# Performance work log

Measured on AMD Instinct MI355X. Metric: run time of the kernel, lower is better.

## Reference

```python
import jax, jax.numpy as jnp
import numpy as np

N_NODES = 100000
E2 = 1600000
E3 = 1600000
ES = 100000
HID = 64


def _mlp_3x3(x_in, W1, b1, W2, b2):
    # x_in: [E, d_in] -> mobility [E, 3, 3]
    h = jax.nn.relu(x_in @ W1 + b1)
    out = h @ W2 + b2  # [E, 9]
    return out.reshape(-1, 3, 3)


def setup_inputs() -> dict:
    key = jax.random.key(0)
    ks = jax.random.split(key, 20)
    inp = {}
    inp["x"] = jax.random.normal(ks[0], (N_NODES, 3), dtype=jnp.float32)
    inp["edge_2body"] = jax.random.randint(ks[1], (2, E2), 0, N_NODES)
    inp["edge_3body"] = jax.random.randint(ks[2], (3, E3), 0, N_NODES)
    inp["edge_2bodySelf"] = jax.random.randint(ks[3], (2, ES), 0, N_NODES)
    inp["edge_1body"] = jax.random.randint(ks[4], (2, ES), 0, N_NODES)
    inp["edge_attr_2body"] = jax.random.normal(ks[5], (E2, 3), dtype=jnp.float32)
    inp["edge_attr_3body"] = jax.random.normal(ks[6], (E3, 3), dtype=jnp.float32)
    inp["edge_attr_2bodySelf"] = jax.random.normal(ks[7], (ES, 3), dtype=jnp.float32)
    inp["edge_attr_1body"] = jax.random.normal(ks[8], (ES, 3), dtype=jnp.float32)
    s = 0.1
    # nn_2body: 3 -> HID -> 9
    inp["W1_2b"] = jax.random.normal(ks[9], (3, HID), dtype=jnp.float32) * s
    inp["b1_2b"] = jnp.zeros((HID,), jnp.float32)
    inp["W2_2b"] = jax.random.normal(ks[10], (HID, 9), dtype=jnp.float32) * s
    inp["b2_2b"] = jnp.zeros((9,), jnp.float32)
    # nn_3body: 6 -> HID -> 9
    inp["W1_3b"] = jax.random.normal(ks[11], (6, HID), dtype=jnp.float32) * s
    inp["b1_3b"] = jnp.zeros((HID,), jnp.float32)
    inp["W2_3b"] = jax.random.normal(ks[12], (HID, 9), dtype=jnp.float32) * s
    inp["b2_3b"] = jnp.zeros((9,), jnp.float32)
    # nn_self: 3 -> HID -> 9
    inp["W1_s"] = jax.random.normal(ks[13], (3, HID), dtype=jnp.float32) * s
    inp["b1_s"] = jnp.zeros((HID,), jnp.float32)
    inp["W2_s"] = jax.random.normal(ks[14], (HID, 9), dtype=jnp.float32) * s
    inp["b2_s"] = jnp.zeros((9,), jnp.float32)
    return inp


def reference(x, edge_2body, edge_3body, edge_2bodySelf, edge_1body,
              edge_attr_2body, edge_attr_3body, edge_attr_2bodySelf, edge_attr_1body,
              W1_2b, b1_2b, W2_2b, b2_2b,
              W1_3b, b1_3b, W2_3b, b2_3b,
              W1_s, b1_s, W2_s, b2_s):
    n = x.shape[0]
    # ---- 2-body: gather -> MLP -> per-edge 3x3 matvec -> scatter-add ----
    d2 = x[edge_2body[0]] - x[edge_2body[1]]  # xj - xi, [E2,3]
    mob2 = _mlp_3x3(d2, W1_2b, b1_2b, W2_2b, b2_2b)
    y2 = jnp.einsum('eij,ej->ei', mob2, edge_attr_2body)
    v2 = jax.ops.segment_sum(y2, edge_2body[1], num_segments=n)
    # ---- 3-body ----
    xj = x[edge_3body[0]]
    xk = x[edge_3body[1]]
    xi = x[edge_3body[2]]
    d3 = jnp.concatenate((xk - xj, xi - xk), axis=1)  # [E3,6]
    mob3 = _mlp_3x3(d3, W1_3b, b1_3b, W2_3b, b2_3b)
    y3 = jnp.einsum('eij,ej->ei', mob3, edge_attr_3body)
    v3 = jax.ops.segment_sum(y3, edge_3body[2], num_segments=n)
    # ---- 2-body self ----
    ds = x[edge_2bodySelf[0]] - x[edge_2bodySelf[1]]
    mobs = _mlp_3x3(ds, W1_s, b1_s, W2_s, b2_s)
    ys = jnp.einsum('eij,ej->ei', mobs, edge_attr_2bodySelf)
    vs = jax.ops.segment_sum(ys, edge_2bodySelf[1], num_segments=n)
    # edge_1body / edge_attr_1body unused in original forward
    return v2 + v3 + vs
```

## Files before the change

kernel.cpp:

```cpp
#include <hip/hip_runtime.h>


constexpr int HIDDEN = 64;
constexpr int NB_MAX = 256;
constexpr int NPB_SHIFT = 9;
constexpr int NPB = 1 << NPB_SHIFT;
constexpr int SSPLIT = 8;
constexpr int TILE_F = NPB * 3;
constexpr int TILE_F4 = TILE_F / 4;
constexpr int NET_SLOT = 1024;
constexpr int NET_USED = 640;

typedef _Float16 h2_t __attribute__((ext_vector_type(2)));

__device__ __forceinline__ unsigned packh2(float a, float b) {
    auto h = __builtin_amdgcn_cvt_pkrtz(a, b);
    return __builtin_bit_cast(unsigned, h);
}
__device__ __forceinline__ float fdot2u(unsigned a, unsigned b, float c) {
    h2_t ha = __builtin_bit_cast(h2_t, a);
    h2_t hb = __builtin_bit_cast(h2_t, b);
#if __has_builtin(__builtin_amdgcn_fdot2)
    return __builtin_amdgcn_fdot2(ha, hb, c, false);
#else
    return fmaf((float)ha.x, (float)hb.x, fmaf((float)ha.y, (float)hb.y, c));
#endif
}


__global__ __launch_bounds__(256) void setup_kernel(
    const float* __restrict__ x, int n_nodes, float4* __restrict__ x4,
    int* __restrict__ gcount,
    const float* __restrict__ W1_2b, const float* __restrict__ b1_2b,
    const float* __restrict__ W2_2b, const float* __restrict__ b2_2b,
    const float* __restrict__ W1_s,  const float* __restrict__ b1_s,
    const float* __restrict__ W2_s,  const float* __restrict__ b2_s,
    const float* __restrict__ W1_3b, const float* __restrict__ b1_3b,
    const float* __restrict__ W2_3b, const float* __restrict__ b2_3b,
    unsigned* __restrict__ nets)
{
    const int blk = blockIdx.x;
    const int tid = threadIdx.x;
    if (blk < 3) {
        const float *W1, *b1, *W2, *b2; int din;
        if (blk == 0) { W1 = W1_2b; b1 = b1_2b; W2 = W2_2b; b2 = b2_2b; din = 3; }
        else if (blk == 1) { W1 = W1_s; b1 = b1_s; W2 = W2_s; b2 = b2_s; din = 3; }
        else { W1 = W1_3b; b1 = b1_3b; W2 = W2_3b; b2 = b2_3b; din = 6; }
        unsigned* slot = nets + blk * NET_SLOT;
        float* slotf = (float*)slot;
        if (tid < 64) {
            int hh = tid;
            if (din == 3) {
                slot[hh] = packh2(W1[0 * HIDDEN + hh], W1[1 * HIDDEN + hh]);
                slotf[560 + hh] = W1[2 * HIDDEN + hh];
            } else {
                #pragma unroll
                for (int r = 0; r < 3; ++r)
                    slot[hh * 3 + r] =
                        packh2(W1[(2 * r) * HIDDEN + hh], W1[(2 * r + 1) * HIDDEN + hh]);
            }
            slotf[192 + hh] = b1[hh];
        }
        for (int t = tid; t < 288; t += 256) {
            int hh2 = t / 9, i = t - hh2 * 9;
            slot[256 + t] = packh2(W2[(2 * hh2) * 9 + i], W2[(2 * hh2 + 1) * 9 + i]);
        }
        if (tid < 9) slotf[544 + tid] = b2[tid];
        if (blk == 0) gcount[tid] = 0;
    } else {
        int i = (blk - 3) * 256 + tid;
        if (i < n_nodes)
            x4[i] = make_float4(x[3 * i], x[3 * i + 1], x[3 * i + 2], 0.0f);
    }
}

__global__ __launch_bounds__(256) void p1_edge_kernel(
    const float4* __restrict__ x4,
    const int* __restrict__ e0, long long E0, const float* __restrict__ at0,
    const int* __restrict__ e1, long long E1, const float* __restrict__ at1,
    const int* __restrict__ e2, long long E2, const float* __restrict__ at2,
    int g0, int g1,
    const unsigned* __restrict__ nets,
    float4* __restrict__ records, int* __restrict__ gcount, int cap)
{
    constexpr int BLK = 256;
    constexpr int KPT = 4;

    __shared__ int s_hist[NB_MAX];
    __shared__ int s_base[NB_MAX];
    __shared__ int s_rank[NB_MAX];
    __shared__ unsigned s_net[NET_USED];

    const int blk = blockIdx.x;
    const int* edges; long long E; const float* attr;
    int bidx, nblk, din3;
    const unsigned* wp;
    if (blk < g0)           { edges = e0; E = E0; attr = at0; bidx = blk;          nblk = g0;                 din3 = 1; wp = nets; }
    else if (blk < g0 + g1) { edges = e1; E = E1; attr = at1; bidx = blk - g0;     nblk = g1;                 din3 = 1; wp = nets + NET_SLOT; }
    else                    { edges = e2; E = E2; attr = at2; bidx = blk - g0 - g1; nblk = gridDim.x - g0 - g1; din3 = 0; wp = nets + 2 * NET_SLOT; }

    const int tid = threadIdx.x;
    const long long span = (E + nblk - 1) / nblk;
    const long long lo = (long long)bidx * span;
    const long long hi = (lo + span < E) ? (lo + span) : E;
    if (lo >= E) return;

    for (int i = tid; i < NB_MAX; i += BLK) { s_hist[i] = 0; s_rank[i] = 0; }
    for (int i = tid; i < NET_USED; i += BLK) s_net[i] = wp[i];
    __syncthreads();

    const unsigned* w = s_net;
    const float* wf = (const float*)s_net;

    const long long dstrow = din3 ? E : 2 * E;
    for (long long e = lo + tid; e < hi; e += BLK) {
        int d = edges[dstrow + e];
        atomicAdd(&s_hist[d >> NPB_SHIFT], 1);
    }
    __syncthreads();

    for (int i = tid; i < NB_MAX; i += BLK) {
        int h = s_hist[i];
        s_base[i] = (h > 0) ? atomicAdd(&gcount[i], h) : 0;
    }
    __syncthreads();

    for (long long t0 = lo; t0 < hi; t0 += BLK * KPT) {
        unsigned dp[KPT][3];
        float    d2s[KPT];
        float    a[KPT][3];
        int      dst[KPT];
        bool     valid[KPT];

        #pragma unroll
        for (int u = 0; u < KPT; ++u) {
            long long e = t0 + (long long)u * BLK + tid;
            valid[u] = (e < hi);
            long long ee = valid[u] ? e : lo;
            if (din3) {
                int s = edges[ee];
                int t = edges[E + ee];
                dst[u] = t;
                float4 xs = x4[s];
                float4 xt = x4[t];
                dp[u][0] = packh2(xs.x - xt.x, xs.y - xt.y);
                d2s[u]   = xs.z - xt.z;
                dp[u][1] = 0; dp[u][2] = 0;
            } else {
                int j = edges[ee];
                int k = edges[E + ee];
                int i = edges[2 * E + ee];
                dst[u] = i;
                float4 xj = x4[j];
                float4 xk = x4[k];
                float4 xi = x4[i];
                dp[u][0] = packh2(xk.x - xj.x, xk.y - xj.y);
                dp[u][1] = packh2(xk.z - xj.z, xi.x - xk.x);
                dp[u][2] = packh2(xi.y - xk.y, xi.z - xk.z);
                d2s[u] = 0.f;
            }
            #pragma unroll
            for (int c = 0; c < 3; ++c) a[u][c] = attr[3 * ee + c];
        }

        float acc[KPT][9];
        #pragma unroll
        for (int u = 0; u < KPT; ++u)
            #pragma unroll
            for (int i = 0; i < 9; ++i) acc[u][i] = wf[544 + i];

        if (din3) {
            #pragma unroll 2
            for (int hh2 = 0; hh2 < HIDDEN / 2; ++hh2) {
                const unsigned wA = w[2 * hh2];
                const unsigned wB = w[2 * hh2 + 1];
                const float wcA = wf[560 + 2 * hh2];
                const float wcB = wf[561 + 2 * hh2];
                const float bbA = wf[192 + 2 * hh2];
                const float bbB = wf[193 + 2 * hh2];
                unsigned w2p[9];
                #pragma unroll
                for (int i = 0; i < 9; ++i) w2p[i] = w[256 + hh2 * 9 + i];
                #pragma unroll
                for (int u = 0; u < KPT; ++u) {
                    float preA = fmaf(d2s[u], wcA, fdot2u(dp[u][0], wA, bbA));
                    float preB = fmaf(d2s[u], wcB, fdot2u(dp[u][0], wB, bbB));
                    unsigned h2 = packh2(fmaxf(preA, 0.f), fmaxf(preB, 0.f));
                    #pragma unroll
                    for (int i = 0; i < 9; ++i)
                        acc[u][i] = fdot2u(h2, w2p[i], acc[u][i]);
                }
            }
        } else {
            #pragma unroll 2
            for (int hh2 = 0; hh2 < HIDDEN / 2; ++hh2) {
                const unsigned wA0 = w[(2 * hh2) * 3 + 0];
                const unsigned wA1 = w[(2 * hh2) * 3 + 1];
                const unsigned wA2 = w[(2 * hh2) * 3 + 2];
                const unsigned wB0 = w[(2 * hh2 + 1) * 3 + 0];
                const unsigned wB1 = w[(2 * hh2 + 1) * 3 + 1];
                const unsigned wB2 = w[(2 * hh2 + 1) * 3 + 2];
                const float bbA = wf[192 + 2 * hh2];
                const float bbB = wf[193 + 2 * hh2];
                unsigned w2p[9];
                #pragma unroll
                for (int i = 0; i < 9; ++i) w2p[i] = w[256 + hh2 * 9 + i];
                #pragma unroll
                for (int u = 0; u < KPT; ++u) {
                    float preA = fdot2u(dp[u][2], wA2,
                                 fdot2u(dp[u][1], wA1,
                                 fdot2u(dp[u][0], wA0, bbA)));
                    float preB = fdot2u(dp[u][2], wB2,
                                 fdot2u(dp[u][1], wB1,
                                 fdot2u(dp[u][0], wB0, bbB)));
                    unsigned h2 = packh2(fmaxf(preA, 0.f), fmaxf(preB, 0.f));
                    #pragma unroll
                    for (int i = 0; i < 9; ++i)
                        acc[u][i] = fdot2u(h2, w2p[i], acc[u][i]);
                }
            }
        }

        #pragma unroll
        for (int u = 0; u < KPT; ++u) {
            if (!valid[u]) continue;
            float y0 = fmaf(acc[u][0], a[u][0], fmaf(acc[u][1], a[u][1], acc[u][2] * a[u][2]));
            float y1 = fmaf(acc[u][3], a[u][0], fmaf(acc[u][4], a[u][1], acc[u][5] * a[u][2]));
            float y2 = fmaf(acc[u][6], a[u][0], fmaf(acc[u][7], a[u][1], acc[u][8] * a[u][2]));
            int b = dst[u] >> NPB_SHIFT;
            int r = atomicAdd(&s_rank[b], 1);
            int slot = s_base[b] + r;
            if (slot < cap)
                records[(size_t)b * cap + slot] =
                    make_float4(y0, y1, y2, __int_as_float(dst[u]));
        }
    }
}

__global__ __launch_bounds__(256) void p2_partial(
    const float4* __restrict__ records, const int* __restrict__ gcount,
    int cap, float* __restrict__ partials)
{
    __shared__ float s_acc[TILE_F];
    const int b = blockIdx.x / SSPLIT;
    const int s = blockIdx.x % SSPLIT;
    const int tid = threadIdx.x;

    for (int i = tid; i < TILE_F; i += 256) s_acc[i] = 0.0f;
    __syncthreads();

    int cnt = gcount[b];
    if (cnt > cap) cnt = cap;
    const int chunk = (cnt + SSPLIT - 1) / SSPLIT;
    const int beg = s * chunk;
    const int end = min(beg + chunk, cnt);

    const float4* rb = records + (size_t)b * cap;
    for (int i = beg + tid; i < end; i += 256) {
        float4 r = rb[i];
        int loc = __float_as_int(r.w) - (b << NPB_SHIFT);
        atomicAdd(&s_acc[loc * 3 + 0], r.x);
        atomicAdd(&s_acc[loc * 3 + 1], r.y);
        atomicAdd(&s_acc[loc * 3 + 2], r.z);
    }
    __syncthreads();

    float* pt = partials + (size_t)blockIdx.x * TILE_F;
    for (int i = tid; i < TILE_F; i += 256) pt[i] = s_acc[i];
}

__global__ __launch_bounds__(256) void p2_final(
    const float4* __restrict__ partials, float4* __restrict__ out, int n4)
{
    int i4 = blockIdx.x * 256 + threadIdx.x;
    if (i4 >= n4) return;
    int b = i4 / TILE_F4;
    int loc = i4 - b * TILE_F4;
    const float4* base = partials + (size_t)b * SSPLIT * TILE_F4 + loc;
    float4 sum = base[0];
    #pragma unroll
    for (int s = 1; s < SSPLIT; ++s) {
        float4 v = base[(size_t)s * TILE_F4];
        sum.x += v.x; sum.y += v.y; sum.z += v.z; sum.w += v.w;
    }
    out[i4] = sum;
}

__global__ void p2_final_tail(const float* __restrict__ partials,
                              float* __restrict__ out, int start, int n)
{
    int idx = start + blockIdx.x * 64 + threadIdx.x;
    if (idx >= n) return;
    int b = idx / TILE_F;
    int loc = idx - b * TILE_F;
    const float* base = partials + (size_t)b * SSPLIT * TILE_F + loc;
    float sum = 0.f;
    #pragma unroll
    for (int s = 0; s < SSPLIT; ++s) sum += base[(size_t)s * TILE_F];
    out[idx] = sum;
}

template <int DIN, int KPT>
__global__ __launch_bounds__(256) void edge_mlp_atomic(
    const float* __restrict__ x,
    const int* __restrict__ edges, long long E,
    const float* __restrict__ attr,
    const float* __restrict__ W1, const float* __restrict__ b1,
    const float* __restrict__ W2, const float* __restrict__ b2,
    float* __restrict__ out)
{
    const int tid = threadIdx.x;
    const long long base = (long long)blockIdx.x * (blockDim.x * KPT) + tid;
    float d[KPT][DIN]; float a[KPT][3]; int dst[KPT]; bool valid[KPT];
    #pragma unroll
    for (int u = 0; u < KPT; ++u) {
        long long e = base + (long long)u * blockDim.x;
        valid[u] = (e < E);
        long long ee = valid[u] ? e : 0;
        if constexpr (DIN == 3) {
            int s = edges[ee]; int t = edges[E + ee]; dst[u] = t;
            #pragma unroll
            for (int c = 0; c < 3; ++c)
                d[u][c] = x[3 * (long long)s + c] - x[3 * (long long)t + c];
        } else {
            int j = edges[ee]; int k = edges[E + ee]; int i = edges[2 * E + ee];
            dst[u] = i;
            #pragma unroll
            for (int c = 0; c < 3; ++c) {
                float xj = x[3 * (long long)j + c];
                float xk = x[3 * (long long)k + c];
                float xi = x[3 * (long long)i + c];
                d[u][c] = xk - xj; d[u][3 + c] = xi - xk;
            }
        }
        #pragma unroll
        for (int c = 0; c < 3; ++c) a[u][c] = attr[3 * ee + c];
    }
    float acc[KPT][9];
    #pragma unroll
    for (int u = 0; u < KPT; ++u)
        #pragma unroll
        for (int i = 0; i < 9; ++i) acc[u][i] = b2[i];
    #pragma unroll 4
    for (int hh = 0; hh < HIDDEN; ++hh) {
        const float bb = b1[hh];
        float w1r[DIN];
        #pragma unroll
        for (int r = 0; r < DIN; ++r) w1r[r] = W1[r * HIDDEN + hh];
        float w2r[9];
        #pragma unroll
        for (int i = 0; i < 9; ++i) w2r[i] = W2[hh * 9 + i];
        #pragma unroll
        for (int u = 0; u < KPT; ++u) {
            float pre = bb;
            #pragma unroll
            for (int r = 0; r < DIN; ++r) pre = fmaf(d[u][r], w1r[r], pre);
            const float h = fmaxf(pre, 0.0f);
            #pragma unroll
            for (int i = 0; i < 9; ++i) acc[u][i] = fmaf(h, w2r[i], acc[u][i]);
        }
    }
    #pragma unroll
    for (int u = 0; u < KPT; ++u) {
        if (!valid[u]) continue;
        float* o = out + 3 * (long long)dst[u];
        #pragma unroll
        for (int i = 0; i < 3; ++i) {
            float y = fmaf(acc[u][3 * i + 0], a[u][0],
                      fmaf(acc[u][3 * i + 1], a[u][1],
                           acc[u][3 * i + 2] * a[u][2]));
            atomicAdd(&o[i], y);
        }
    }
}

extern "C" void kernel_launch(void* const* d_in, const int* in_sizes, int n_in,
                              void* d_out, int out_size, void* d_ws, size_t ws_size,
                              hipStream_t stream)
{
    const float* x  = (const float*)d_in[0];
    const int*   e2 = (const int*)d_in[1];
    const int*   e3 = (const int*)d_in[2];
    const int*   es = (const int*)d_in[3];
    const float* a2 = (const float*)d_in[5];
    const float* a3 = (const float*)d_in[6];
    const float* as = (const float*)d_in[7];
    const float* W1_2b = (const float*)d_in[9];
    const float* b1_2b = (const float*)d_in[10];
    const float* W2_2b = (const float*)d_in[11];
    const float* b2_2b = (const float*)d_in[12];
    const float* W1_3b = (const float*)d_in[13];
    const float* b1_3b = (const float*)d_in[14];
    const float* W2_3b = (const float*)d_in[15];
    const float* b2_3b = (const float*)d_in[16];
    const float* W1_s  = (const float*)d_in[17];
    const float* b1_s  = (const float*)d_in[18];
    const float* W2_s  = (const float*)d_in[19];
    const float* b2_s  = (const float*)d_in[20];

    const long long E2 = in_sizes[1] / 2;
    const long long E3 = in_sizes[2] / 3;
    const long long ES = in_sizes[3] / 2;
    const long long Etot = E2 + E3 + ES;
    const int n_nodes = out_size / 3;
    const int nbuckets = (n_nodes + NPB - 1) >> NPB_SHIFT;

    float* out = (float*)d_out;

    const size_t off_nets = 1024;
    const size_t off_x4 = off_nets + 3 * NET_SLOT * 4;
    const size_t x4_bytes = (size_t)n_nodes * sizeof(float4);
    const size_t off_part = (off_x4 + x4_bytes + 255) & ~(size_t)255;
    const size_t part_bytes = (size_t)nbuckets * SSPLIT * TILE_F * sizeof(float);
    const size_t off_rec = off_part + part_bytes;

    long long mean_per_bucket = (Etot + nbuckets - 1) / nbuckets;
    long long min_cap = mean_per_bucket + 1600;
    long long cap_avail =
        ((long long)ws_size - (long long)off_rec) / ((long long)nbuckets * 16);

    constexpr int SPAN = 2048;
    int g0 = (int)((E2 + SPAN - 1) / SPAN);
    int g1 = (int)((ES + SPAN - 1) / SPAN);
    int g2g = (int)((E3 + SPAN - 1) / SPAN);

    if (nbuckets <= NB_MAX && cap_avail >= min_cap) {
        long long capL = min_cap + 4096;
        if (capL > cap_avail) capL = cap_avail;
        int cap = (int)capL;
        int* gcount = (int*)d_ws;
        unsigned* nets = (unsigned*)((char*)d_ws + off_nets);
        float4* x4 = (float4*)((char*)d_ws + off_x4);
        float* partials = (float*)((char*)d_ws + off_part);
        float4* records = (float4*)((char*)d_ws + off_rec);

        int nb_pad = (n_nodes + 255) / 256;
        setup_kernel<<<3 + nb_pad, 256, 0, stream>>>(
            x, n_nodes, x4, gcount,
            W1_2b, b1_2b, W2_2b, b2_2b,
            W1_s,  b1_s,  W2_s,  b2_s,
            W1_3b, b1_3b, W2_3b, b2_3b,
            nets);

        p1_edge_kernel<<<g0 + g1 + g2g, 256, 0, stream>>>(
            x4,
            e2, E2, a2,
            es, ES, as,
            e3, E3, a3,
            g0, g1,
            nets, records, gcount, cap);

        p2_partial<<<nbuckets * SSPLIT, 256, 0, stream>>>(records, gcount, cap, partials);

        int n4 = out_size / 4;
        int tail = out_size - n4 * 4;
        if (n4 > 0)
            p2_final<<<(n4 + 255) / 256, 256, 0, stream>>>(
                (const float4*)partials, (float4*)out, n4);
        if (tail > 0)
            p2_final_tail<<<1, 64, 0, stream>>>(partials, out, n4 * 4, out_size);
    } else {
        hipMemsetAsync(out, 0, (size_t)out_size * sizeof(float), stream);
        constexpr int BLK = 256, KPT = 4;
        const long long per_blk = (long long)BLK * KPT;
        int a2g = (int)((E2 + per_blk - 1) / per_blk);
        int a3g = (int)((E3 + per_blk - 1) / per_blk);
        int asg = (int)((ES + per_blk - 1) / per_blk);
        if (a2g > 0)
            edge_mlp_atomic<3, KPT><<<a2g, BLK, 0, stream>>>(
                x, e2, E2, a2, W1_2b, b1_2b, W2_2b, b2_2b, out);
        if (a3g > 0)
            edge_mlp_atomic<6, KPT><<<a3g, BLK, 0, stream>>>(
                x, e3, E3, a3, W1_3b, b1_3b, W2_3b, b2_3b, out);
        if (asg > 0)
            edge_mlp_atomic<3, KPT><<<asg, BLK, 0, stream>>>(
                x, es, ES, as, W1_s, b1_s, W2_s, b2_s, out);
    }
}
```

Measured before the change: 325.3 us.

## Reduce each bucket in one 1024-thread block and write output directly

Replaces the split per-bucket partial reduction (8 blocks per bucket writing partials) and the separate final-sum kernels with a single 1024-thread block per bucket that accumulates in shared memory and writes straight to the output. This drops one kernel launch and the partials round trip through global memory. The cost is fewer blocks (about 196 for 100k nodes), each serially processing all records of its bucket, which lowers parallelism across the GPU's compute units.

Result: no change. 325.7 us (+0.1%).

```diff
diff --git a/kernel.cpp b/kernel.cpp
--- a/kernel.cpp
+++ b/kernel.cpp
@@ -5,9 +5,7 @@
 constexpr int NB_MAX = 256;
 constexpr int NPB_SHIFT = 9;
 constexpr int NPB = 1 << NPB_SHIFT;
-constexpr int SSPLIT = 8;
 constexpr int TILE_F = NPB * 3;
-constexpr int TILE_F4 = TILE_F / 4;
 constexpr int NET_SLOT = 1024;
 constexpr int NET_USED = 640;
 
@@ -237,26 +235,21 @@
     }
 }
 
-__global__ __launch_bounds__(256) void p2_partial(
+__global__ __launch_bounds__(1024) void p2_bucket(
     const float4* __restrict__ records, const int* __restrict__ gcount,
-    int cap, float* __restrict__ partials)
+    int cap, int n_nodes, float* __restrict__ out)
 {
     __shared__ float s_acc[TILE_F];
-    const int b = blockIdx.x / SSPLIT;
-    const int s = blockIdx.x % SSPLIT;
+    const int b = blockIdx.x;
     const int tid = threadIdx.x;
 
-    for (int i = tid; i < TILE_F; i += 256) s_acc[i] = 0.0f;
+    for (int i = tid; i < TILE_F; i += 1024) s_acc[i] = 0.0f;
     __syncthreads();
 
     int cnt = gcount[b];
     if (cnt > cap) cnt = cap;
-    const int chunk = (cnt + SSPLIT - 1) / SSPLIT;
-    const int beg = s * chunk;
-    const int end = min(beg + chunk, cnt);
-
     const float4* rb = records + (size_t)b * cap;
-    for (int i = beg + tid; i < end; i += 256) {
+    for (int i = tid; i < cnt; i += 1024) {
         float4 r = rb[i];
         int loc = __float_as_int(r.w) - (b << NPB_SHIFT);
         atomicAdd(&s_acc[loc * 3 + 0], r.x);
@@ -265,39 +258,10 @@
     }
     __syncthreads();
 
-    float* pt = partials + (size_t)blockIdx.x * TILE_F;
-    for (int i = tid; i < TILE_F; i += 256) pt[i] = s_acc[i];
-}
-
-__global__ __launch_bounds__(256) void p2_final(
-    const float4* __restrict__ partials, float4* __restrict__ out, int n4)
-{
-    int i4 = blockIdx.x * 256 + threadIdx.x;
-    if (i4 >= n4) return;
-    int b = i4 / TILE_F4;
-    int loc = i4 - b * TILE_F4;
-    const float4* base = partials + (size_t)b * SSPLIT * TILE_F4 + loc;
-    float4 sum = base[0];
-    #pragma unroll
-    for (int s = 1; s < SSPLIT; ++s) {
-        float4 v = base[(size_t)s * TILE_F4];
-        sum.x += v.x; sum.y += v.y; sum.z += v.z; sum.w += v.w;
-    }
-    out[i4] = sum;
-}
-
-__global__ void p2_final_tail(const float* __restrict__ partials,
-                              float* __restrict__ out, int start, int n)
-{
-    int idx = start + blockIdx.x * 64 + threadIdx.x;
-    if (idx >= n) return;
-    int b = idx / TILE_F;
-    int loc = idx - b * TILE_F;
-    const float* base = partials + (size_t)b * SSPLIT * TILE_F + loc;
-    float sum = 0.f;
-    #pragma unroll
-    for (int s = 0; s < SSPLIT; ++s) sum += base[(size_t)s * TILE_F];
-    out[idx] = sum;
+    const int start = (b << NPB_SHIFT) * 3;
+    const int end = min(n_nodes * 3, ((b + 1) << NPB_SHIFT) * 3);
+    for (int i = start + tid; i < end; i += 1024)
+        out[i] = s_acc[i - start];
 }
 
 template <int DIN, int KPT>
@@ -410,9 +374,7 @@
     const size_t off_nets = 1024;
     const size_t off_x4 = off_nets + 3 * NET_SLOT * 4;
     const size_t x4_bytes = (size_t)n_nodes * sizeof(float4);
-    const size_t off_part = (off_x4 + x4_bytes + 255) & ~(size_t)255;
-    const size_t part_bytes = (size_t)nbuckets * SSPLIT * TILE_F * sizeof(float);
-    const size_t off_rec = off_part + part_bytes;
+    const size_t off_rec = (off_x4 + x4_bytes + 255) & ~(size_t)255;
 
     long long mean_per_bucket = (Etot + nbuckets - 1) / nbuckets;
     long long min_cap = mean_per_bucket + 1600;
@@ -431,7 +393,6 @@
         int* gcount = (int*)d_ws;
         unsigned* nets = (unsigned*)((char*)d_ws + off_nets);
         float4* x4 = (float4*)((char*)d_ws + off_x4);
-        float* partials = (float*)((char*)d_ws + off_part);
         float4* records = (float4*)((char*)d_ws + off_rec);
 
         int nb_pad = (n_nodes + 255) / 256;
@@ -450,15 +411,7 @@
             g0, g1,
             nets, records, gcount, cap);
 
-        p2_partial<<<nbuckets * SSPLIT, 256, 0, stream>>>(records, gcount, cap, partials);
-
-        int n4 = out_size / 4;
-        int tail = out_size - n4 * 4;
-        if (n4 > 0)
-            p2_final<<<(n4 + 255) / 256, 256, 0, stream>>>(
-                (const float4*)partials, (float4*)out, n4);
-        if (tail > 0)
-            p2_final_tail<<<1, 64, 0, stream>>>(partials, out, n4 * 4, out_size);
+        p2_bucket<<<nbuckets, 1024, 0, stream>>>(records, gcount, cap, n_nodes, out);
     } else {
         hipMemsetAsync(out, 0, (size_t)out_size * sizeof(float), stream);
         constexpr int BLK = 256, KPT = 4;
```
